# Kernel tuning notes

Hardware: AMD Instinct MI355X
Metric: run time of the kernel (lower is better)

The kernel has to match this reference:

```python
import jax, jax.numpy as jnp
import numpy as np
from jax import lax

NFEAT = 512      # num_input == RNN hidden size
HID = 1000       # autoencoder hidden width
BSZ = 512
T_TOTAL = 65     # num_timesteps + 1 (last step is the forecast target)
MAX_GAP = 16     # t in [1, MAX_GAP]; fixed for jit-compatible decode loop
EPS = 1e-5       # BatchNorm eps


def setup_inputs() -> dict:
    key = jax.random.key(0)
    ks = jax.random.split(key, 24)
    s = 0.02
    n = lambda k, shape: (jax.random.normal(k, shape, jnp.float32) * s)
    inp = {
        "x": jax.random.normal(ks[0], (BSZ, T_TOTAL, NFEAT), jnp.float32),
        "t": jax.random.randint(ks[1], (BSZ,), 1, MAX_GAP + 1),
        # RNN (tanh) cell params, torch layout: W_ih [H, F], W_hh [H, H]
        "W_ih": n(ks[2], (NFEAT, NFEAT)),
        "W_hh": n(ks[3], (NFEAT, NFEAT)),
        "b_ih": n(ks[4], (NFEAT,)),
        "b_hh": n(ks[5], (NFEAT,)),
        # autoenc layer 1: Linear(NFEAT, HID) + BatchNorm1d(HID)
        "W1": n(ks[6], (HID, NFEAT)), "b1": n(ks[7], (HID,)),
        "g1": jax.random.uniform(ks[8], (HID,), jnp.float32, 0.5, 1.5),
        "beta1": n(ks[9], (HID,)),
        "rm1": n(ks[10], (HID,)),
        "rv1": jax.random.uniform(ks[11], (HID,), jnp.float32, 0.5, 1.5),
        # autoenc layer 2: Linear(HID, HID) + BatchNorm1d(HID)
        "W2": n(ks[12], (HID, HID)), "b2": n(ks[13], (HID,)),
        "g2": jax.random.uniform(ks[14], (HID,), jnp.float32, 0.5, 1.5),
        "beta2": n(ks[15], (HID,)),
        "rm2": n(ks[16], (HID,)),
        "rv2": jax.random.uniform(ks[17], (HID,), jnp.float32, 0.5, 1.5),
        # autoenc layer 3: Linear(HID, NFEAT) + BatchNorm1d(NFEAT)
        "W3": n(ks[18], (NFEAT, HID)), "b3": n(ks[19], (NFEAT,)),
        "g3": jax.random.uniform(ks[20], (NFEAT,), jnp.float32, 0.5, 1.5),
        "beta3": n(ks[21], (NFEAT,)),
        "rm3": n(ks[22], (NFEAT,)),
        "rv3": jax.random.uniform(ks[23], (NFEAT,), jnp.float32, 0.5, 1.5),
    }
    return inp


def reference(x, t, W_ih, W_hh, b_ih, b_hh,
              W1, b1, g1, beta1, rm1, rv1,
              W2, b2, g2, beta2, rm2, rv2,
              W3, b3, g3, beta3, rm3, rv3):
    def bn(z, g, b, rm, rv):
        # eval-mode BatchNorm1d (running stats); Dropout is identity in eval
        return (z - rm) * (g * lax.rsqrt(rv + EPS)) + b

    def autoenc(h):  # h: [N, NFEAT]
        z = bn(h @ W1.T + b1, g1, beta1, rm1, rv1)
        z = bn(z @ W2.T + b2, g2, beta2, rm2, rv2)
        z = bn(z @ W3.T + b3, g3, beta3, rm3, rv3)
        return z

    def cell(xt, h):  # single tanh RNN step
        return jnp.tanh(xt @ W_ih.T + b_ih + h @ W_hh.T + b_hh)

    x_final = x[:, -1, :]           # [B, F]
    xin = x[:, :-1, :]              # [B, T, F]
    B, T, F = xin.shape

    # encode: run RNN over the observed sequence (h0 = 0)
    def step(h, xt):
        h2 = cell(xt, h)
        return h2, h2
    h0 = jnp.zeros((B, F), xin.dtype)
    _, hs = lax.scan(step, h0, jnp.swapaxes(xin, 0, 1))  # [T, B, F]
    h = jnp.swapaxes(hs, 0, 1)                           # [B, T, F]

    y = autoenc(h.reshape(B * T, F)).reshape(B, T, F)

    # one-step-ahead reconstruction loss: MSE * (1/nelement)
    nelt1 = (T - 1) * B * F
    lossval = jnp.mean((y[:, :-1, :] - xin[:, 1:, :]) ** 2) / nelt1

    def dec(carry, _):
        h_hat, x_hat = carry
        h2 = cell(x_hat, h_hat)
        x2 = autoenc(h2)
        return (h2, x2), x2
    (_, _), xs = lax.scan(dec, (h[:, -1, :], y[:, -1, :]), None, length=MAX_GAP)
    x_all_gaps = jnp.swapaxes(xs, 0, 1)                  # [B, MAX_GAP, F]

    gap = (t - 1).astype(jnp.int32)                      # per-sample index
    x_pred = jnp.take_along_axis(x_all_gaps, gap[:, None, None], axis=1)[:, 0, :]

    nelt2 = B * F
    lossval = lossval + jnp.mean((x_pred - x_final) ** 2) / nelt2
    return x_pred, lossval
```

## Files before the change

### kernel.cpp

```cpp
#include <hip/hip_runtime.h>
#include <math.h>


typedef unsigned short ushort_t;
typedef __attribute__((ext_vector_type(8))) short short8;
typedef __attribute__((ext_vector_type(4))) float f32x4;

#define BB 512
#define TT 65
#define TN 64
#define FF 512
#define HD 1000
#define HDP 1024
#define EPSBN 1e-5f
#define BF (BB*FF)
#define MALL (BB*TN)
#define HP 520
#define RROWS 8
#define WLS 136

__device__ __forceinline__ ushort_t f2bf(float f) {
    union { float f; unsigned u; } v; v.f = f;
    unsigned r = v.u + 0x7FFFu + ((v.u >> 16) & 1u);
    return (ushort_t)(r >> 16);
}

__device__ __forceinline__ float b2f(ushort_t u) {
    union { unsigned u; float f; } v; v.u = ((unsigned)u) << 16;
    return v.f;
}

__device__ __forceinline__ float ftanh(float x) {
    const float e = __expf(2.f * x);
    return 1.f - 2.f / (e + 1.f);
}

__device__ __forceinline__ void ld16(const ushort_t* g, ushort_t* l) {
    __builtin_amdgcn_global_load_lds(
        (const __attribute__((address_space(1))) unsigned*)g,
        (__attribute__((address_space(3))) unsigned*)l, 16, 0, 0);
}

__global__ __launch_bounds__(256)
void mfma_gemm(const ushort_t* __restrict__ A, long a_rs,
               const ushort_t* __restrict__ W, int K, int Nreal,
               void* __restrict__ outv, long o_rs,
               const float* __restrict__ aux, int epi, int mbase,
               const float* __restrict__ p1, const float* __restrict__ p2,
               const float* __restrict__ rv, const float* __restrict__ gg,
               ushort_t* __restrict__ out2, float* __restrict__ sums)
{
    __shared__ ushort_t As[128 * 32];
    __shared__ ushort_t Bs[128 * 32];
    __shared__ float red[256];

    const int tid  = threadIdx.x;
    const int wave = tid >> 6, lane = tid & 63;
    const int wm = wave >> 1, wn = wave & 1;
    const int tileM = blockIdx.y * 128, tileN = blockIdx.x * 128;

    f32x4 acc[4][4] = {};
    const int srow = lane >> 2;
    const int skb  = (lane & 3) * 8;

    for (int kt = 0; kt < K; kt += 32) {
        __syncthreads();
#pragma unroll
        for (int s = 0; s < 2; ++s) {
            const int instr = wave * 2 + s;
            const int row = instr * 16 + srow;
            ld16(A + (size_t)(tileM + row) * a_rs + kt + skb, &As[instr * 512]);
            ld16(W + (size_t)(tileN + row) * (size_t)K + kt + skb, &Bs[instr * 512]);
        }
        __syncthreads();
        const int lr = lane & 15;
        const int lk = (lane >> 4) * 8;
        short8 af[4], bfr[4];
#pragma unroll
        for (int i = 0; i < 4; ++i)
            af[i] = *(const short8*)&As[(wm * 64 + i * 16 + lr) * 32 + lk];
#pragma unroll
        for (int j = 0; j < 4; ++j)
            bfr[j] = *(const short8*)&Bs[(wn * 64 + j * 16 + lr) * 32 + lk];
#pragma unroll
        for (int i = 0; i < 4; ++i)
#pragma unroll
            for (int j = 0; j < 4; ++j)
                acc[i][j] = __builtin_amdgcn_mfma_f32_16x16x32_bf16(
                    af[i], bfr[j], acc[i][j], 0, 0, 0);
    }

    const int lr = lane & 15;
    const int rquad = (lane >> 4) * 4;
    float lsum = 0.f;
#pragma unroll
    for (int i = 0; i < 4; ++i) {
#pragma unroll
        for (int r = 0; r < 4; ++r) {
            const int grow = tileM + wm * 64 + i * 16 + rquad + r;
#pragma unroll
            for (int j = 0; j < 4; ++j) {
                const int gcol = tileN + wn * 64 + j * 16 + lr;
                const float v = acc[i][j][r];
                if (epi == 0) {
                    ((float*)outv)[(size_t)grow * o_rs + gcol] = v + p1[gcol] + p2[gcol];
                } else if (epi == 1) {
                    ((ushort_t*)outv)[(size_t)grow * o_rs + gcol] = f2bf(v);
                } else if (epi == 6) {
                    const float w0 = b2f(out2[(size_t)grow * o_rs + gcol]);
                    ((ushort_t*)outv)[(size_t)grow * o_rs + gcol] = f2bf(v + w0);
                } else if (epi == 7) {
                    ((float*)outv)[(size_t)grow * o_rs + gcol] = v + p1[gcol];
                } else if (epi == 8) {
                    float o = 0.f;
                    if (gcol < Nreal)
                        o = v * (gg[gcol] * rsqrtf(rv[gcol] + EPSBN));
                    ((ushort_t*)outv)[(size_t)grow * o_rs + gcol] = f2bf(o);
                } else {
                    const float o = v + p1[gcol];
                    const int gm = mbase + grow;
                    const int b = gm >> 6, tau = gm & 63;
                    if (tau < 63) {
                        const float d = o - aux[((size_t)b * TT + tau + 1) * FF + gcol];
                        lsum += d * d;
                    } else {
                        out2[(size_t)b * FF + gcol] = f2bf(o);
                    }
                }
            }
        }
    }
    if (epi == 5) {
        red[tid] = lsum;
        __syncthreads();
        for (int o = 128; o > 0; o >>= 1) {
            if (tid < o) red[tid] += red[tid + o];
            __syncthreads();
        }
        if (tid == 0) atomicAdd(&sums[0], red[0]);
    }
}

__global__ __launch_bounds__(512, 2)
void rnn_persistent(const ushort_t* __restrict__ Whh,
                    const float* __restrict__ XW,
                    ushort_t* __restrict__ hs)
{
    __shared__ ushort_t hb[2][RROWS * HP];
    __shared__ ushort_t wl[8 * 64 * WLS];
    const int tid = threadIdx.x, wave = tid >> 6, lane = tid & 63;
    const int b0 = blockIdx.x * RROWS;
    const int lr = lane & 15, lq = lane >> 4;
    const int rq = lq * 4;
    const int c0 = wave * 64;
    ushort_t* wlw = wl + wave * (64 * WLS);

    short8 wreg[12][4];
#pragma unroll
    for (int kc = 0; kc < 12; ++kc)
#pragma unroll
        for (int nt = 0; nt < 4; ++nt)
            wreg[kc][nt] = *(const short8*)(Whh +
                (size_t)(c0 + nt * 16 + lr) * FF + kc * 32 + lq * 8);
#pragma unroll
    for (int i = 0; i < 16; ++i) {
        const int u = i * 64 + lane;
        const int row = u >> 4, c16 = u & 15;
        *(uint4*)&wlw[row * WLS + c16 * 8] =
            *(const uint4*)(Whh + (size_t)(c0 + row) * FF + 384 + c16 * 8);
    }

#pragma unroll
    for (int it = 0; it < 2; ++it) {
        const int e = (it * 512 + tid) * 4;
        const int row = e >> 9, col = e & 511;
        const size_t gi = ((size_t)(b0 + row) * TN) * FF + col;
        const float4 v = *(const float4*)&XW[gi];
        const ushort_t h0 = f2bf(ftanh(v.x)), h1 = f2bf(ftanh(v.y));
        const ushort_t h2 = f2bf(ftanh(v.z)), h3 = f2bf(ftanh(v.w));
        hb[0][row * HP + col + 0] = h0; hb[0][row * HP + col + 1] = h1;
        hb[0][row * HP + col + 2] = h2; hb[0][row * HP + col + 3] = h3;
        unsigned r0 = (unsigned)h0 | ((unsigned)h1 << 16);
        unsigned r1 = (unsigned)h2 | ((unsigned)h3 << 16);
        *(uint2*)&hs[gi] = make_uint2(r0, r1);
    }
    __syncthreads();

    f32x4 acc[4];
    short8 af[3];

    for (int t = 1; t < TN; ++t) {
        const ushort_t* hcur = hb[(t - 1) & 1];
#pragma unroll
        for (int s = 0; s < 2; ++s)
            af[s] = *(const short8*)&hcur[(lr & 7) * HP + s * 32 + lq * 8];
#pragma unroll
        for (int j = 0; j < 4; ++j) acc[j] = (f32x4){0.f, 0.f, 0.f, 0.f};

#pragma unroll
        for (int kc = 0; kc < 16; ++kc) {
            if (kc + 2 < 16)
                af[(kc + 2) % 3] = *(const short8*)
                    &hcur[(lr & 7) * HP + (kc + 2) * 32 + lq * 8];
            const int b = kc % 3;
            if (kc < 12) {
#pragma unroll
                for (int nt = 0; nt < 4; ++nt)
                    acc[nt] = __builtin_amdgcn_mfma_f32_16x16x32_bf16(
                        af[b], wreg[kc][nt], acc[nt], 0, 0, 0);
            } else {
#pragma unroll
                for (int nt = 0; nt < 4; ++nt) {
                    const short8 wfr = *(const short8*)
                        &wlw[(nt * 16 + lr) * WLS + (kc - 12) * 32 + lq * 8];
                    acc[nt] = __builtin_amdgcn_mfma_f32_16x16x32_bf16(
                        af[b], wfr, acc[nt], 0, 0, 0);
                }
            }
        }

        ushort_t* hnxt = hb[t & 1];
        if (rq < 8) {
#pragma unroll
            for (int nt = 0; nt < 4; ++nt) {
                const int col = c0 + nt * 16 + lr;
#pragma unroll
                for (int r = 0; r < 4; ++r) {
                    const int row = rq + r;
                    const size_t gi = ((size_t)(b0 + row) * TN + t) * FF + col;
                    const ushort_t hv = f2bf(ftanh(acc[nt][r] + XW[gi]));
                    hnxt[row * HP + col] = hv;
                    hs[gi] = hv;
                }
            }
        }
        __syncthreads();
    }
}

__global__ __launch_bounds__(256)
void decode_fused(const ushort_t* __restrict__ Wf,
                  const float* __restrict__ bfv,
                  const ushort_t* __restrict__ hs,
                  ushort_t* __restrict__ hall)
{
    __shared__ ushort_t hb[2][16 * HP];
    const int tid = threadIdx.x, wave = tid >> 6, lane = tid & 63;
    const int b0 = blockIdx.x * 16;
    const int lr = lane & 15, lq = lane >> 4;
    const int c0 = wave * 128;

    for (int it = 0; it < 4; ++it) {
        const int e = (it * 256 + tid) * 8;
        const int row = e >> 9, col = e & 511;
        const uint4 v = *(const uint4*)&hs[((size_t)(b0 + row) * TN + 63) * FF + col];
        *(uint4*)&hb[0][row * HP + col] = v;
    }
    __syncthreads();

    float bfj[8];
#pragma unroll
    for (int j = 0; j < 8; ++j) bfj[j] = bfv[c0 + j * 16 + lr];

    f32x4 acc[8];
    short8 wf[3][8];
    short8 af[3];

    for (int g = 0; g < 16; ++g) {
        const ushort_t* hcur = hb[g & 1];
#pragma unroll
        for (int s = 0; s < 2; ++s) {
            const int kk = s * 32 + lq * 8;
            af[s] = *(const short8*)&hcur[lr * HP + kk];
#pragma unroll
            for (int j = 0; j < 8; ++j)
                wf[s][j] = *(const short8*)(Wf + (size_t)(c0 + j * 16 + lr) * FF + kk);
        }
#pragma unroll
        for (int j = 0; j < 8; ++j) acc[j] = (f32x4){0.f, 0.f, 0.f, 0.f};

#pragma unroll
        for (int kc = 0; kc < 16; ++kc) {
            if (kc + 2 < 16) {
                const int slot = (kc + 2) % 3;
                const int kk = (kc + 2) * 32 + lq * 8;
                af[slot] = *(const short8*)&hcur[lr * HP + kk];
#pragma unroll
                for (int j = 0; j < 8; ++j)
                    wf[slot][j] = *(const short8*)
                        (Wf + (size_t)(c0 + j * 16 + lr) * FF + kk);
            }
            const int b = kc % 3;
#pragma unroll
            for (int j = 0; j < 8; ++j)
                acc[j] = __builtin_amdgcn_mfma_f32_16x16x32_bf16(
                    af[b], wf[b][j], acc[j], 0, 0, 0);
        }

        ushort_t* hnxt = hb[(g + 1) & 1];
#pragma unroll
        for (int j = 0; j < 8; ++j) {
            const int col = c0 + j * 16 + lr;
#pragma unroll
            for (int r = 0; r < 4; ++r) {
                const int row = lq * 4 + r;
                const ushort_t hv = f2bf(ftanh(acc[j][r] + bfj[j]));
                hnxt[row * HP + col] = hv;
                hall[((size_t)g * BB + b0 + row) * FF + col] = hv;
            }
        }
        __syncthreads();
    }
}

__global__ void conv_x(const float* __restrict__ x, ushort_t* __restrict__ xb)
{
    const int i = blockIdx.x * blockDim.x + threadIdx.x;
    if (i < MALL * FF / 4) {
        const int e = i * 4;
        const int m = e >> 9;
        const int f = e & (FF - 1);
        const int b = m >> 6, t = m & 63;
        const float4 v = *(const float4*)&x[((size_t)b * TT + t) * FF + f];
        unsigned r0 = (unsigned)f2bf(v.x) | ((unsigned)f2bf(v.y) << 16);
        unsigned r1 = (unsigned)f2bf(v.z) | ((unsigned)f2bf(v.w) << 16);
        *(uint2*)&xb[e] = make_uint2(r0, r1);
    }
}

__global__ void conv_w(const float* __restrict__ src, ushort_t* __restrict__ dst,
                       int Nsrc, int Ksrc, int Npad, int Kpad)
{
    const int i = blockIdx.x * blockDim.x + threadIdx.x;
    if (i < Npad * Kpad) {
        const int n = i / Kpad, k = i - n * Kpad;
        const float v = (n < Nsrc && k < Ksrc) ? src[(size_t)n * Ksrc + k] : 0.f;
        dst[i] = f2bf(v);
    }
}

__global__ void conv_m1t(const float* __restrict__ W1,
                         const float* __restrict__ g1,
                         const float* __restrict__ rv1,
                         ushort_t* __restrict__ M1T)
{
    const int i = blockIdx.x * blockDim.x + threadIdx.x;
    if (i < FF * HDP) {
        const int k = i >> 10, j = i & (HDP - 1);
        float v = 0.f;
        if (j < HD)
            v = g1[j] * rsqrtf(rv1[j] + EPSBN) * W1[(size_t)j * FF + k];
        M1T[i] = f2bf(v);
    }
}

__global__ void conv_w3s(const float* __restrict__ W3,
                         const float* __restrict__ g3,
                         const float* __restrict__ rv3,
                         ushort_t* __restrict__ dst)
{
    const int i = blockIdx.x * blockDim.x + threadIdx.x;
    if (i < FF * HDP) {
        const int n = i >> 10, k = i & (HDP - 1);
        float v = 0.f;
        if (k < HD)
            v = g3[n] * rsqrtf(rv3[n] + EPSBN) * W3[(size_t)n * HD + k];
        dst[i] = f2bf(v);
    }
}

__global__ void fuse_c1(const float* __restrict__ b1, const float* __restrict__ rm1,
                        const float* __restrict__ rv1, const float* __restrict__ g1,
                        const float* __restrict__ be1, float* __restrict__ c1)
{
    const int j = blockIdx.x * blockDim.x + threadIdx.x;
    if (j < HDP) {
        float o = 0.f;
        if (j < HD) {
            const float s = g1[j] * rsqrtf(rv1[j] + EPSBN);
            o = (b1[j] - rm1[j]) * s + be1[j];
        }
        c1[j] = o;
    }
}

__global__ void fuse_mv(const float* __restrict__ W, int K, int Mreal,
                        const float* __restrict__ vin,
                        const float* __restrict__ gg, const float* __restrict__ rv,
                        const float* __restrict__ bb, const float* __restrict__ rm,
                        const float* __restrict__ be,
                        const float* __restrict__ a1, const float* __restrict__ a2,
                        float* __restrict__ out, int Mout)
{
    const int i = blockIdx.x * blockDim.x + threadIdx.x;
    if (i >= Mout) return;
    float o = 0.f;
    if (i < Mreal) {
        const float* row = W + (size_t)i * K;
        float d = 0.f;
        for (int j = 0; j < K; ++j) d += row[j] * vin[j];
        if (gg) {
            const float s = gg[i] * rsqrtf(rv[i] + EPSBN);
            o = s * d + (bb[i] - rm[i]) * s + be[i];
        } else {
            o = d + a1[i] + a2[i];
        }
    }
    out[i] = o;
}

__global__ void zero_init(float* __restrict__ sums)
{
    if (threadIdx.x < 2 && blockIdx.x == 0) sums[threadIdx.x] = 0.f;
}

__global__ void gather_kernel(const float* __restrict__ xgaps,
                              const int* __restrict__ tgap,
                              const float* __restrict__ x,
                              float* __restrict__ out,
                              float* __restrict__ sums)
{
    const int i = blockIdx.x * blockDim.x + threadIdx.x;
    float s = 0.f;
    if (i < BF) {
        const int b = i >> 9, f = i & (FF - 1);
        const int g = tgap[b] - 1;
        const float v = xgaps[((size_t)g * BB + b) * FF + f];
        out[i] = v;
        const float d = v - x[((size_t)b * TT + (TT - 1)) * FF + f];
        s = d * d;
    }
    __shared__ float red[256];
    red[threadIdx.x] = s;
    __syncthreads();
    for (int o = 128; o > 0; o >>= 1) {
        if (threadIdx.x < o) red[threadIdx.x] += red[threadIdx.x + o];
        __syncthreads();
    }
    if (threadIdx.x == 0) atomicAdd(&sums[1], red[0]);
}

__global__ void finalize_kernel(const float* __restrict__ sums,
                                float* __restrict__ out)
{
    if (threadIdx.x == 0 && blockIdx.x == 0) {
        const double n1 = 63.0 * 512.0 * 512.0;
        const double n2 = 512.0 * 512.0;
        out[BF] = (float)((double)sums[0] / (n1 * n1) +
                          (double)sums[1] / (n2 * n2));
    }
}

extern "C" void kernel_launch(void* const* d_in, const int* in_sizes, int n_in,
                              void* d_out, int out_size, void* d_ws, size_t ws_size,
                              hipStream_t stream)
{
    const float* x    = (const float*)d_in[0];
    const int*   tgap = (const int*)d_in[1];
    const float* W_ih = (const float*)d_in[2];
    const float* W_hh = (const float*)d_in[3];
    const float* b_ih = (const float*)d_in[4];
    const float* b_hh = (const float*)d_in[5];
    const float* W1 = (const float*)d_in[6];
    const float* b1 = (const float*)d_in[7];
    const float* g1 = (const float*)d_in[8];
    const float* be1 = (const float*)d_in[9];
    const float* rm1 = (const float*)d_in[10];
    const float* rv1 = (const float*)d_in[11];
    const float* W2 = (const float*)d_in[12];
    const float* b2 = (const float*)d_in[13];
    const float* g2 = (const float*)d_in[14];
    const float* be2 = (const float*)d_in[15];
    const float* rm2 = (const float*)d_in[16];
    const float* rv2 = (const float*)d_in[17];
    const float* W3 = (const float*)d_in[18];
    const float* b3 = (const float*)d_in[19];
    const float* g3 = (const float*)d_in[20];
    const float* be3 = (const float*)d_in[21];
    const float* rm3 = (const float*)d_in[22];
    const float* rv3 = (const float*)d_in[23];
    float* out = (float*)d_out;

    char* p = (char*)d_ws;
    auto take = [&](size_t bytes) -> char* {
        char* r = p; p += (bytes + 63) & ~(size_t)63; return r;
    };
    float*    XWbuf = (float*)take((size_t)MALL * FF * 4);
    ushort_t* hs    = (ushort_t*)take((size_t)MALL * FF * 2);
    ushort_t* xbf   = (ushort_t*)take((size_t)MALL * FF * 2);
    float*    xg    = (float*)take((size_t)16 * BF * 4);
    ushort_t* hall  = (ushort_t*)take((size_t)16 * BF * 2);
    ushort_t* seed  = (ushort_t*)take((size_t)BF * 2);
    ushort_t* Wihb  = (ushort_t*)take((size_t)FF * FF * 2);
    ushort_t* Whhb  = (ushort_t*)take((size_t)FF * FF * 2);
    ushort_t* W2b   = (ushort_t*)take((size_t)HDP * HDP * 2);
    ushort_t* W3s   = (ushort_t*)take((size_t)FF * HDP * 2);
    ushort_t* M1T   = (ushort_t*)take((size_t)FF * HDP * 2);
    ushort_t* Tts   = (ushort_t*)take((size_t)FF * HDP * 2);
    ushort_t* Anb   = (ushort_t*)take((size_t)FF * FF * 2);
    ushort_t* At    = (ushort_t*)take((size_t)FF * FF * 2);
    ushort_t* Wfb   = (ushort_t*)take((size_t)FF * FF * 2);
    float*    c1v   = (float*)take((size_t)HDP * 4);
    float*    v2v   = (float*)take((size_t)HDP * 4);
    float*    bAv   = (float*)take((size_t)FF * 4);
    float*    bfv   = (float*)take((size_t)FF * 4);
    float*    sums  = (float*)take(16 * 4);

    const dim3 blk(256);

    zero_init<<<dim3(1), dim3(64), 0, stream>>>(sums);
    conv_x<<<dim3(MALL * FF / 4 / 256), blk, 0, stream>>>(x, xbf);
    conv_w<<<dim3((FF * FF + 255) / 256), blk, 0, stream>>>(W_ih, Wihb, FF, FF, FF, FF);
    conv_w<<<dim3((FF * FF + 255) / 256), blk, 0, stream>>>(W_hh, Whhb, FF, FF, FF, FF);
    conv_w<<<dim3((HDP * HDP + 255) / 256), blk, 0, stream>>>(W2, W2b, HD, HD, HDP, HDP);
    conv_w3s<<<dim3((FF * HDP + 255) / 256), blk, 0, stream>>>(W3, g3, rv3, W3s);
    conv_m1t<<<dim3((FF * HDP + 255) / 256), blk, 0, stream>>>(W1, g1, rv1, M1T);

    fuse_c1<<<dim3((HDP + 255) / 256), blk, 0, stream>>>(b1, rm1, rv1, g1, be1, c1v);
    fuse_mv<<<dim3((HDP + 255) / 256), blk, 0, stream>>>(
        W2, HD, HD, c1v, g2, rv2, b2, rm2, be2, nullptr, nullptr, v2v, HDP);
    fuse_mv<<<dim3((FF + 255) / 256), blk, 0, stream>>>(
        W3, HD, FF, v2v, g3, rv3, b3, rm3, be3, nullptr, nullptr, bAv, FF);
    fuse_mv<<<dim3((FF + 255) / 256), blk, 0, stream>>>(
        W_ih, FF, FF, bAv, nullptr, nullptr, nullptr, nullptr, nullptr,
        b_ih, b_hh, bfv, FF);

    mfma_gemm<<<dim3(HDP / 128, FF / 128), blk, 0, stream>>>(
        M1T, HDP, W2b, HDP, HD, Tts, HDP, nullptr, 8, 0,
        nullptr, nullptr, rv2, g2, nullptr, nullptr);
    mfma_gemm<<<dim3(FF / 128, FF / 128), blk, 0, stream>>>(
        W3s, HDP, Tts, HDP, FF, Anb, FF, nullptr, 1, 0,
        nullptr, nullptr, nullptr, nullptr, nullptr, nullptr);
    mfma_gemm<<<dim3(FF / 128, FF / 128), blk, 0, stream>>>(
        Tts, HDP, W3s, HDP, FF, At, FF, nullptr, 1, 0,
        nullptr, nullptr, nullptr, nullptr, nullptr, nullptr);
    mfma_gemm<<<dim3(FF / 128, FF / 128), blk, 0, stream>>>(
        Wihb, FF, At, FF, FF, Wfb, FF, nullptr, 6, 0,
        nullptr, nullptr, nullptr, nullptr, Whhb, nullptr);

    mfma_gemm<<<dim3(FF / 128, MALL / 128), blk, 0, stream>>>(
        xbf, FF, Wihb, FF, FF, XWbuf, FF, nullptr, 0, 0,
        b_ih, b_hh, nullptr, nullptr, nullptr, nullptr);
    rnn_persistent<<<dim3(BB / RROWS), dim3(512), 0, stream>>>(Whhb, XWbuf, hs);

    mfma_gemm<<<dim3(FF / 128, MALL / 128), blk, 0, stream>>>(
        hs, FF, Anb, FF, FF, nullptr, 0, x, 5, 0,
        bAv, nullptr, nullptr, nullptr, seed, sums);

    decode_fused<<<dim3(BB / 16), blk, 0, stream>>>(Wfb, bfv, hs, hall);

    mfma_gemm<<<dim3(FF / 128, (16 * BB) / 128), blk, 0, stream>>>(
        hall, FF, Anb, FF, FF, xg, FF, nullptr, 7, 0,
        bAv, nullptr, nullptr, nullptr, nullptr, nullptr);

    gather_kernel<<<dim3(BF / 256), blk, 0, stream>>>(xg, tgap, x, out, sums);
    finalize_kernel<<<dim3(1), dim3(64), 0, stream>>>(sums, out);
}
```

Before: 1.376 ms.

## Rebalance RNN epilogue across all lanes, swizzle LDS weights, split t0 init

```diff
diff --git a/kernel.cpp b/kernel.cpp
--- a/kernel.cpp
+++ b/kernel.cpp
@@ -17,7 +17,7 @@
 #define MALL (BB*TN)
 #define HP 520
 #define RROWS 8
-#define WLS 136
+#define WLS 128
 
 __device__ __forceinline__ ushort_t f2bf(float f) {
     union { float f; unsigned u; } v; v.f = f;
@@ -141,7 +141,21 @@
     }
 }
 
-__global__ __launch_bounds__(512, 2)
+__global__ void rnn_t0(const float* __restrict__ XW, ushort_t* __restrict__ hs)
+{
+    const int i = blockIdx.x * blockDim.x + threadIdx.x;
+    if (i < BF / 2) {
+        const int b = i / (FF / 2), c = (i - b * (FF / 2)) * 2;
+        const size_t g = ((size_t)b * TN) * FF + c;
+        const float2 v = *(const float2*)&XW[g];
+        const unsigned rr = (unsigned)f2bf(ftanh(v.x)) |
+                            ((unsigned)f2bf(ftanh(v.y)) << 16);
+        *(unsigned*)&hs[g] = rr;
+    }
+}
+
+__global__ __launch_bounds__(512)
+__attribute__((amdgpu_waves_per_eu(2, 2)))
 void rnn_persistent(const ushort_t* __restrict__ Whh,
                     const float* __restrict__ XW,
                     ushort_t* __restrict__ hs)
@@ -151,7 +165,6 @@
     const int tid = threadIdx.x, wave = tid >> 6, lane = tid & 63;
     const int b0 = blockIdx.x * RROWS;
     const int lr = lane & 15, lq = lane >> 4;
-    const int rq = lq * 4;
     const int c0 = wave * 64;
     ushort_t* wlw = wl + wave * (64 * WLS);
 
@@ -162,35 +175,36 @@
         for (int nt = 0; nt < 4; ++nt)
             wreg[kc][nt] = *(const short8*)(Whh +
                 (size_t)(c0 + nt * 16 + lr) * FF + kc * 32 + lq * 8);
+
 #pragma unroll
     for (int i = 0; i < 16; ++i) {
         const int u = i * 64 + lane;
         const int row = u >> 4, c16 = u & 15;
-        *(uint4*)&wlw[row * WLS + c16 * 8] =
+        const int boff = (row * (WLS * 2) + c16 * 16) ^ ((row & 7) << 4);
+        *(uint4*)((char*)wlw + boff) =
             *(const uint4*)(Whh + (size_t)(c0 + row) * FF + 384 + c16 * 8);
     }
 
-#pragma unroll
-    for (int it = 0; it < 2; ++it) {
-        const int e = (it * 512 + tid) * 4;
-        const int row = e >> 9, col = e & 511;
-        const size_t gi = ((size_t)(b0 + row) * TN) * FF + col;
-        const float4 v = *(const float4*)&XW[gi];
-        const ushort_t h0 = f2bf(ftanh(v.x)), h1 = f2bf(ftanh(v.y));
-        const ushort_t h2 = f2bf(ftanh(v.z)), h3 = f2bf(ftanh(v.w));
-        hb[0][row * HP + col + 0] = h0; hb[0][row * HP + col + 1] = h1;
-        hb[0][row * HP + col + 2] = h2; hb[0][row * HP + col + 3] = h3;
-        unsigned r0 = (unsigned)h0 | ((unsigned)h1 << 16);
-        unsigned r1 = (unsigned)h2 | ((unsigned)h3 << 16);
-        *(uint2*)&hs[gi] = make_uint2(r0, r1);
+    {
+        const int r2 = tid >> 6, cu = (tid & 63) * 8;
+        *(uint4*)&hb[0][r2 * HP + cu] =
+            *(const uint4*)&hs[((size_t)(b0 + r2) * TN) * FF + cu];
     }
     __syncthreads();
+
+    const int base_r = (lq & 1) * 4 + (lq >> 1) * 2;
+    const float*  xwp0 = XW + ((size_t)(b0 + base_r) * TN) * FF + c0 + lr;
+    const float*  xwp1 = XW + ((size_t)(b0 + base_r + 1) * TN) * FF + c0 + lr;
+    ushort_t*     hsp0 = hs + ((size_t)(b0 + base_r) * TN) * FF + c0 + lr;
+    ushort_t*     hsp1 = hs + ((size_t)(b0 + base_r + 1) * TN) * FF + c0 + lr;
+    const int hbo = base_r * HP + c0 + lr;
 
     f32x4 acc[4];
     short8 af[3];
 
     for (int t = 1; t < TN; ++t) {
         const ushort_t* hcur = hb[(t - 1) & 1];
+        xwp0 += FF; xwp1 += FF; hsp0 += FF; hsp1 += FF;
 #pragma unroll
         for (int s = 0; s < 2; ++s)
             af[s] = *(const short8*)&hcur[(lr & 7) * HP + s * 32 + lq * 8];
@@ -211,27 +225,26 @@
             } else {
 #pragma unroll
                 for (int nt = 0; nt < 4; ++nt) {
-                    const short8 wfr = *(const short8*)
-                        &wlw[(nt * 16 + lr) * WLS + (kc - 12) * 32 + lq * 8];
+                    const int boff = (((nt * 16 + lr) * WLS +
+                                       (kc - 12) * 32 + lq * 8) * 2)
+                                     ^ ((lr & 7) << 4);
+                    const short8 wfr = *(const short8*)((char*)wlw + boff);
                     acc[nt] = __builtin_amdgcn_mfma_f32_16x16x32_bf16(
                         af[b], wfr, acc[nt], 0, 0, 0);
                 }
             }
         }
 
-        ushort_t* hnxt = hb[t & 1];
-        if (rq < 8) {
-#pragma unroll
-            for (int nt = 0; nt < 4; ++nt) {
-                const int col = c0 + nt * 16 + lr;
-#pragma unroll
-                for (int r = 0; r < 4; ++r) {
-                    const int row = rq + r;
-                    const size_t gi = ((size_t)(b0 + row) * TN + t) * FF + col;
-                    const ushort_t hv = f2bf(ftanh(acc[nt][r] + XW[gi]));
-                    hnxt[row * HP + col] = hv;
-                    hs[gi] = hv;
-                }
+        ushort_t* hn = hb[t & 1];
+#pragma unroll
+        for (int nt = 0; nt < 4; ++nt) {
+#pragma unroll
+            for (int j = 0; j < 2; ++j) {
+                const float a = (lq & 2) ? acc[nt][2 + j] : acc[nt][j];
+                const float xv = j ? xwp1[nt * 16] : xwp0[nt * 16];
+                const ushort_t hv = f2bf(ftanh(a + xv));
+                hn[hbo + j * HP + nt * 16] = hv;
+                if (j) hsp1[nt * 16] = hv; else hsp0[nt * 16] = hv;
             }
         }
         __syncthreads();
@@ -541,6 +554,7 @@
     mfma_gemm<<<dim3(FF / 128, MALL / 128), blk, 0, stream>>>(
         xbf, FF, Wihb, FF, FF, XWbuf, FF, nullptr, 0, 0,
         b_ih, b_hh, nullptr, nullptr, nullptr, nullptr);
+    rnn_t0<<<dim3(BF / 2 / 256), blk, 0, stream>>>(XWbuf, hs);
     rnn_persistent<<<dim3(BB / RROWS), dim3(512), 0, stream>>>(Whhb, XWbuf, hs);
 
     mfma_gemm<<<dim3(FF / 128, MALL / 128), blk, 0, stream>>>(
```

Measured after the change: 1.111 ms. -19.2%, faster.
